# Performance work log

Measured on AMD Instinct MI355X. Metric: run time of the kernel, lower is better.

## Reference

```python
import jax, jax.numpy as jnp
import numpy as np
import math

D_MODEL = 1024
N_HEAD = 16


def setup_inputs() -> dict:
    key = jax.random.key(0)
    ks = jax.random.split(key, 5)
    x = jax.random.normal(ks[0], (2, 2048, D_MODEL), dtype=jnp.float32)
    # Linear params (torch Linear: y = x @ W.T + b); store as [in, out] for einsum
    s1 = 1.0 / math.sqrt(D_MODEL)
    W_qkv = jax.random.uniform(ks[1], (D_MODEL, 3 * D_MODEL), jnp.float32, -s1, s1)
    b_qkv = jax.random.uniform(ks[2], (3 * D_MODEL,), jnp.float32, -s1, s1)
    W_out = jax.random.uniform(ks[3], (D_MODEL, D_MODEL), jnp.float32, -s1, s1)
    b_out = jax.random.uniform(ks[4], (D_MODEL,), jnp.float32, -s1, s1)
    return {"x": x, "W_qkv": W_qkv, "b_qkv": b_qkv, "W_out": W_out, "b_out": b_out}


def reference(x, W_qkv, b_qkv, W_out, b_out):
    B, L, D = x.shape
    H = N_HEAD
    hd = D // H
    qkv = x @ W_qkv + b_qkv                      # [B, L, 3D]
    q, k, v = jnp.split(qkv, 3, axis=-1)
    # [B, H, L, hd]
    q = q.reshape(B, L, H, hd).transpose(0, 2, 1, 3)
    k = k.reshape(B, L, H, hd).transpose(0, 2, 1, 3)
    v = v.reshape(B, L, H, hd).transpose(0, 2, 1, 3)
    scale = 1.0 / math.sqrt(hd)
    scores = jnp.einsum('bhqd,bhkd->bhqk', q, k) * scale   # [B, H, L, L]
    causal = jnp.tril(jnp.ones((L, L), dtype=bool))
    scores = jnp.where(causal, scores, jnp.float32(-jnp.inf))
    probs = jax.nn.softmax(scores, axis=-1)
    out = jnp.einsum('bhqk,bhkd->bhqd', probs, v)          # [B, H, L, hd]
    out = out.transpose(0, 2, 1, 3).reshape(B, L, D)
    out = out @ W_out + b_out
    return jnp.squeeze(out)
```

## Files before the change

kernel.cpp:

```cpp
#include <hip/hip_runtime.h>
#include <hip/hip_bf16.h>

#define SEQ    2048
#define NHEAD  16
#define HD     64
#define DMODEL 1024

using bf16 = __hip_bfloat16;
using short8 = __attribute__((ext_vector_type(8))) short;
using short4v = __attribute__((ext_vector_type(4))) short;
using f32x4  = __attribute__((ext_vector_type(4))) float;

__device__ __forceinline__ float fast_exp2(float x) {
  return __builtin_amdgcn_exp2f(x);
}
#define WAIT_LGKM0() __builtin_amdgcn_s_waitcnt(0xC07F)

__device__ __forceinline__ void gload_lds16(const bf16* g, bf16* l) {
  __builtin_amdgcn_global_load_lds(
      (const __attribute__((address_space(1))) void*)g,
      (__attribute__((address_space(3))) void*)l, 16, 0, 0);
}


__global__ void prep_k(const float* __restrict__ x, bf16* __restrict__ xb,
                       const float* __restrict__ Wqkv, bf16* __restrict__ WqkvT,
                       const float* __restrict__ Wout, bf16* __restrict__ WoutT) {
  __shared__ bf16 tile[32][33];
  const int id = blockIdx.x, tid = threadIdx.x;
  if (id < 2048) {
    int i = (id * 256 + tid) * 8;
    bf16 tmp[8];
    #pragma unroll
    for (int j = 0; j < 8; ++j) tmp[j] = __float2bfloat16(x[i + j]);
    *(short8*)&xb[i] = *(short8*)tmp;
    return;
  }
  const float* in; bf16* out; int R, C, tx32, ty32;
  if (id < 2048 + 3072) {
    int t = id - 2048; in = Wqkv; out = WqkvT; R = 1024; C = 3072;
    tx32 = t % 96; ty32 = t / 96;
  } else {
    int t = id - 5120; in = Wout; out = WoutT; R = 1024; C = 1024;
    tx32 = t % 32; ty32 = t / 32;
  }
  int c0 = tx32 * 32, r0 = ty32 * 32;
  int tx = tid & 31, ty = tid >> 5;
  #pragma unroll
  for (int i = ty; i < 32; i += 8)
    tile[i][tx] = __float2bfloat16(in[(size_t)(r0 + i) * C + c0 + tx]);
  __syncthreads();
  #pragma unroll
  for (int i = ty; i < 32; i += 8)
    out[(size_t)(c0 + i) * R + r0 + tx] = tile[tx][i];
}

__global__ void transpose_v_k(const bf16* __restrict__ in, bf16* __restrict__ out) {
  __shared__ bf16 tile[32][33];
  const int bh = blockIdx.z;
  const bf16* ip = in  + (size_t)bh * SEQ * HD;
  bf16* op       = out + (size_t)bh * HD * SEQ;
  int c0 = blockIdx.x * 32, r0 = blockIdx.y * 32;
  int tx = threadIdx.x & 31, ty = threadIdx.x >> 5;
  #pragma unroll
  for (int i = ty; i < 32; i += 8)
    tile[i][tx] = ip[(size_t)(r0 + i) * HD + c0 + tx];
  __syncthreads();
  #pragma unroll
  for (int i = ty; i < 32; i += 8)
    op[(size_t)(c0 + i) * SEQ + r0 + tx] = tile[tx][i];
}

template <int MODE>
__global__ __launch_bounds__(256)
void gemm_bt(const bf16* __restrict__ A, const bf16* __restrict__ BT,
             const float* __restrict__ bias,
             bf16* __restrict__ out0, bf16* __restrict__ out1,
             bf16* __restrict__ out2, float* __restrict__ outf) {
  constexpr int K = 1024;
  __shared__ __align__(16) bf16 As[128 * 32];
  __shared__ __align__(16) bf16 Bs[128 * 32];
  const int tid = threadIdx.x;
  const int wave = tid >> 6, lane = tid & 63;
  const int quad = lane >> 4, l16 = lane & 15;
  const int waveM = (wave >> 1) * 64, waveN = (wave & 1) * 64;
  const int m0 = blockIdx.x * 128, n0 = blockIdx.y * 128;
  const int srow = (lane >> 2);
  const int scol = (((lane & 3) ^ ((lane >> 3) & 3)) * 8);
  const int q8   = (quad ^ ((l16 >> 1) & 3)) * 8;

  const f32x4 zero4 = {0.f, 0.f, 0.f, 0.f};
  f32x4 acc[4][4];
  #pragma unroll
  for (int i = 0; i < 4; ++i)
    #pragma unroll
    for (int j = 0; j < 4; ++j) acc[i][j] = zero4;

  for (int k0 = 0; k0 < K; k0 += 32) {
    __syncthreads();
    #pragma unroll
    for (int half = 0; half < 2; ++half) {
      int grow = half * 64 + wave * 16 + srow;
      gload_lds16(&A [(size_t)(m0 + grow) * K + k0 + scol],
                  &As[(half * 64 + wave * 16) * 32]);
      gload_lds16(&BT[(size_t)(n0 + grow) * K + k0 + scol],
                  &Bs[(half * 64 + wave * 16) * 32]);
    }
    __syncthreads();
    short8 af[4], bfm[4];
    #pragma unroll
    for (int mt = 0; mt < 4; ++mt)
      af[mt] = *(const short8*)&As[(waveM + mt * 16 + l16) * 32 + q8];
    #pragma unroll
    for (int nt = 0; nt < 4; ++nt)
      bfm[nt] = *(const short8*)&Bs[(waveN + nt * 16 + l16) * 32 + q8];
    #pragma unroll
    for (int mt = 0; mt < 4; ++mt)
      #pragma unroll
      for (int nt = 0; nt < 4; ++nt)
        acc[mt][nt] = __builtin_amdgcn_mfma_f32_16x16x32_bf16(
            af[mt], bfm[nt], acc[mt][nt], 0, 0, 0);
  }

  #pragma unroll
  for (int nt = 0; nt < 4; ++nt) {
    int n = n0 + waveN + nt * 16 + l16;
    float bvv = bias[n];
    #pragma unroll
    for (int mt = 0; mt < 4; ++mt) {
      #pragma unroll
      for (int r = 0; r < 4; ++r) {
        int m = m0 + waveM + mt * 16 + quad * 4 + r;
        float v = acc[mt][nt][r] + bvv;
        if (MODE == 1) {
          outf[(size_t)m * 1024 + n] = v;
        } else {
          bf16 v16 = __float2bfloat16(v);
          int which = n >> 10, oo = n & 1023;
          int h = oo >> 6, c = oo & 63;
          int b = m >> 11, l = m & 2047;
          size_t idx = ((size_t)(b * NHEAD + h) * SEQ + l) * HD + c;
          if (which == 0)      out0[idx] = v16;
          else if (which == 1) out1[idx] = v16;
          else                 out2[idx] = v16;
        }
      }
    }
  }
}

__global__ __launch_bounds__(256)
void attn_k(const bf16* __restrict__ Q, const bf16* __restrict__ Kb,
            const bf16* __restrict__ VT, bf16* __restrict__ O) {
  __shared__ __align__(16) bf16 Ks[2][2][64 * 32];
  __shared__ __align__(16) bf16 Vs[2][2][64 * 32];
  __shared__ __align__(16) bf16 Plds[4][16][72];
  const int tid = threadIdx.x;
  const int wave = tid >> 6, lane = tid & 63;
  const int quad = lane >> 4, l16 = lane & 15;
  const int srow = lane >> 2;
  const int scol = (((lane & 3) ^ ((lane >> 3) & 3)) * 8);
  const int q8   = (quad ^ ((l16 >> 1) & 3)) * 8;
  const int id = blockIdx.x;
  const int bh = id & 31, blkx = id >> 5;
  const int b = bh >> 4, h = bh & 15;

  const bf16* Qp = Q  + (size_t)bh * SEQ * HD;
  const bf16* Kp = Kb + (size_t)bh * SEQ * HD;
  const bf16* Vp = VT + (size_t)bh * HD * SEQ;

  const f32x4 zero4 = {0.f, 0.f, 0.f, 0.f};
  const float c = 0.18033688011112042f;
  const float mc = 8.0f * c;

  for (int pass = 0; pass < 2; ++pass) {
    const int qt = pass ? (31 - blkx) : blkx;
    const int q0w = qt * 64 + wave * 16;
    const int q_lane = q0w + l16;
    const int ntiles = qt + 1;

    short8 qf0 = *(const short8*)&Qp[(size_t)(q0w + l16) * HD + quad * 8];
    short8 qf1 = *(const short8*)&Qp[(size_t)(q0w + l16) * HD + 32 + quad * 8];

    f32x4 oacc[4];
    #pragma unroll
    for (int dt = 0; dt < 4; ++dt) oacc[dt] = zero4;
    float l4[4] = {0.f, 0.f, 0.f, 0.f};


    {
      const int k0 = 0;
      #pragma unroll
      for (int hh = 0; hh < 2; ++hh)
        gload_lds16(&Kp[(size_t)(k0 + wave * 16 + srow) * HD + hh * 32 + scol],
                    &Ks[0][hh][(wave * 16) * 32]);
      #pragma unroll
      for (int ch = 0; ch < 2; ++ch)
        gload_lds16(&Vp[(size_t)(wave * 16 + srow) * SEQ + k0 + ch * 32 + scol],
                    &Vs[0][ch][(wave * 16) * 32]);
    }
    __syncthreads();

    for (int t = 0; t < ntiles; ++t) {
      const int buf = t & 1;
      if (t + 1 < ntiles) {
        const int k1 = (t + 1) << 6, nb = buf ^ 1;
        #pragma unroll
        for (int hh = 0; hh < 2; ++hh)
          gload_lds16(&Kp[(size_t)(k1 + wave * 16 + srow) * HD + hh * 32 + scol],
                      &Ks[nb][hh][(wave * 16) * 32]);
        #pragma unroll
        for (int ch = 0; ch < 2; ++ch)
          gload_lds16(&Vp[(size_t)(wave * 16 + srow) * SEQ + k1 + ch * 32 + scol],
                      &Vs[nb][ch][(wave * 16) * 32]);
      }
      const int k0 = t << 6;

      f32x4 s[4];
      #pragma unroll
      for (int g = 0; g < 4; ++g) {
        short8 ka = *(const short8*)&Ks[buf][0][(g * 16 + l16) * 32 + q8];
        short8 kb = *(const short8*)&Ks[buf][1][(g * 16 + l16) * 32 + q8];
        f32x4 sg = zero4;
        sg = __builtin_amdgcn_mfma_f32_16x16x32_bf16(ka, qf0, sg, 0, 0, 0);
        sg = __builtin_amdgcn_mfma_f32_16x16x32_bf16(kb, qf1, sg, 0, 0, 0);
        s[g] = sg;
      }

      if (t == ntiles - 1) {
        #pragma unroll
        for (int g = 0; g < 4; ++g)
          #pragma unroll
          for (int r = 0; r < 4; ++r) {
            int k = k0 + g * 16 + quad * 4 + r;
            s[g][r] = (k <= q_lane) ? s[g][r] : -__builtin_inff();
          }
      }

      #pragma unroll
      for (int g = 0; g < 4; ++g) {
        bf16 pb[4];
        #pragma unroll
        for (int r = 0; r < 4; ++r) {
          float p = fast_exp2(__builtin_fmaf(s[g][r], c, -mc));
          l4[r] += p;
          pb[r] = __float2bfloat16(p);
        }
        *(short4v*)&Plds[wave][l16][g * 16 + quad * 4] = *(short4v*)pb;
      }
      WAIT_LGKM0();

      #pragma unroll
      for (int ch = 0; ch < 2; ++ch) {
        short8 pf = *(const short8*)&Plds[wave][l16][ch * 32 + quad * 8];
        #pragma unroll
        for (int dt = 0; dt < 4; ++dt) {
          short8 vf = *(const short8*)&Vs[buf][ch][(dt * 16 + l16) * 32 + q8];
          oacc[dt] = __builtin_amdgcn_mfma_f32_16x16x32_bf16(vf, pf, oacc[dt], 0, 0, 0);
        }
      }
      __syncthreads();
    }

    float l_i = (l4[0] + l4[1]) + (l4[2] + l4[3]);
    l_i += __shfl_xor(l_i, 16, 64);
    l_i += __shfl_xor(l_i, 32, 64);
    float inv = 1.f / l_i;

    #pragma unroll
    for (int dt = 0; dt < 4; ++dt) {
      bf16 ob[4];
      #pragma unroll
      for (int r = 0; r < 4; ++r) ob[r] = __float2bfloat16(oacc[dt][r] * inv);
      *(short4v*)&Plds[wave][l16][dt * 16 + quad * 4] = *(short4v*)ob;
    }
    WAIT_LGKM0();
    {
      int row = lane >> 2;
      int col = (lane & 3) * 16;
      short8 o0 = *(const short8*)&Plds[wave][row][col];
      short8 o1 = *(const short8*)&Plds[wave][row][col + 8];
      size_t base = ((size_t)(b * SEQ + q0w + row)) * DMODEL + h * HD + col;
      *(short8*)&O[base]     = o0;
      *(short8*)&O[base + 8] = o1;
    }
    WAIT_LGKM0();
  }
}

extern "C" void kernel_launch(void* const* d_in, const int* in_sizes, int n_in,
                              void* d_out, int out_size, void* d_ws, size_t ws_size,
                              hipStream_t stream) {
  const float* x    = (const float*)d_in[0];
  const float* Wqkv = (const float*)d_in[1];
  const float* bqkv = (const float*)d_in[2];
  const float* Wout = (const float*)d_in[3];
  const float* bout = (const float*)d_in[4];
  float* out = (float*)d_out;

  char* ws = (char*)d_ws;
  const size_t MB = 1024 * 1024;
  char* big    = ws + 16384;
  bf16* Kbuf   = (bf16*)(big);
  bf16* VTb    = (bf16*)(big + 8 * MB);
  bf16* xb     = (bf16*)(big + 16 * MB);
  bf16* AO     = (bf16*)(big + 16 * MB);
  bf16* WqkvT  = (bf16*)(big + 24 * MB);
  bf16* WoutT  = (bf16*)(big + 30 * MB);
  bf16* Qb     = (bf16*)d_out;
  bf16* Vtmp   = (bf16*)((char*)d_out + 8 * MB);

  prep_k<<<6144, 256, 0, stream>>>(x, xb, Wqkv, WqkvT, Wout, WoutT);
  gemm_bt<0><<<dim3(4096 / 128, 3072 / 128), 256, 0, stream>>>(
      xb, WqkvT, bqkv, Qb, Kbuf, Vtmp, nullptr);
  transpose_v_k<<<dim3(HD / 32, SEQ / 32, 32), 256, 0, stream>>>(Vtmp, VTb);
  attn_k<<<512, 256, 0, stream>>>(Qb, Kbuf, VTb, AO);
  gemm_bt<1><<<dim3(4096 / 128, 1024 / 128), 256, 0, stream>>>(
      AO, WoutT, bout, nullptr, nullptr, nullptr, out);
}
```

Measured before the change: 178.0 us.

## Fuse V transpose into QKV GEMM epilogue and split attention into one tile per block

The QKV GEMM epilogue now writes V directly in transposed [bh, hd, seq] layout with packed 4-element stores, and the Q/K tiles swap MFMA operands so they can also store 4 contiguous head-dim values. This removes the separate transpose kernel and its extra round trip through memory. The attention kernel drops its two-pass pairing of query tiles, launches 1024 blocks ordered longest-first, and sets launch bounds for 3 blocks per CU plus s_setprio around the MFMA sections. The trade-off is a less even per-block load, and the strided V writes may coalesce poorly.

```diff
diff --git a/kernel.cpp b/kernel.cpp
--- a/kernel.cpp
+++ b/kernel.cpp
@@ -53,22 +53,6 @@
   #pragma unroll
   for (int i = ty; i < 32; i += 8)
     out[(size_t)(c0 + i) * R + r0 + tx] = tile[tx][i];
-}
-
-__global__ void transpose_v_k(const bf16* __restrict__ in, bf16* __restrict__ out) {
-  __shared__ bf16 tile[32][33];
-  const int bh = blockIdx.z;
-  const bf16* ip = in  + (size_t)bh * SEQ * HD;
-  bf16* op       = out + (size_t)bh * HD * SEQ;
-  int c0 = blockIdx.x * 32, r0 = blockIdx.y * 32;
-  int tx = threadIdx.x & 31, ty = threadIdx.x >> 5;
-  #pragma unroll
-  for (int i = ty; i < 32; i += 8)
-    tile[i][tx] = ip[(size_t)(r0 + i) * HD + c0 + tx];
-  __syncthreads();
-  #pragma unroll
-  for (int i = ty; i < 32; i += 8)
-    op[(size_t)(c0 + i) * SEQ + r0 + tx] = tile[tx][i];
 }
 
 template <int MODE>
@@ -85,6 +69,7 @@
   const int quad = lane >> 4, l16 = lane & 15;
   const int waveM = (wave >> 1) * 64, waveN = (wave & 1) * 64;
   const int m0 = blockIdx.x * 128, n0 = blockIdx.y * 128;
+  const bool swapped = (MODE == 0) && (n0 < 2048);
   const int srow = (lane >> 2);
   const int scol = (((lane & 3) ^ ((lane >> 3) & 3)) * 8);
   const int q8   = (quad ^ ((l16 >> 1) & 3)) * 8;
@@ -114,42 +99,80 @@
     #pragma unroll
     for (int nt = 0; nt < 4; ++nt)
       bfm[nt] = *(const short8*)&Bs[(waveN + nt * 16 + l16) * 32 + q8];
-    #pragma unroll
-    for (int mt = 0; mt < 4; ++mt)
-      #pragma unroll
-      for (int nt = 0; nt < 4; ++nt)
-        acc[mt][nt] = __builtin_amdgcn_mfma_f32_16x16x32_bf16(
-            af[mt], bfm[nt], acc[mt][nt], 0, 0, 0);
-  }
-
-  #pragma unroll
-  for (int nt = 0; nt < 4; ++nt) {
-    int n = n0 + waveN + nt * 16 + l16;
-    float bvv = bias[n];
-    #pragma unroll
-    for (int mt = 0; mt < 4; ++mt) {
-      #pragma unroll
-      for (int r = 0; r < 4; ++r) {
-        int m = m0 + waveM + mt * 16 + quad * 4 + r;
-        float v = acc[mt][nt][r] + bvv;
-        if (MODE == 1) {
-          outf[(size_t)m * 1024 + n] = v;
-        } else {
-          bf16 v16 = __float2bfloat16(v);
-          int which = n >> 10, oo = n & 1023;
-          int h = oo >> 6, c = oo & 63;
-          int b = m >> 11, l = m & 2047;
-          size_t idx = ((size_t)(b * NHEAD + h) * SEQ + l) * HD + c;
-          if (which == 0)      out0[idx] = v16;
-          else if (which == 1) out1[idx] = v16;
-          else                 out2[idx] = v16;
+    if (swapped) {
+      #pragma unroll
+      for (int mt = 0; mt < 4; ++mt)
+        #pragma unroll
+        for (int nt = 0; nt < 4; ++nt)
+          acc[mt][nt] = __builtin_amdgcn_mfma_f32_16x16x32_bf16(
+              bfm[nt], af[mt], acc[mt][nt], 0, 0, 0);
+    } else {
+      #pragma unroll
+      for (int mt = 0; mt < 4; ++mt)
+        #pragma unroll
+        for (int nt = 0; nt < 4; ++nt)
+          acc[mt][nt] = __builtin_amdgcn_mfma_f32_16x16x32_bf16(
+              af[mt], bfm[nt], acc[mt][nt], 0, 0, 0);
+    }
+  }
+
+  if (MODE == 1) {
+    #pragma unroll
+    for (int nt = 0; nt < 4; ++nt) {
+      int n = n0 + waveN + nt * 16 + l16;
+      float bvv = bias[n];
+      #pragma unroll
+      for (int mt = 0; mt < 4; ++mt) {
+        #pragma unroll
+        for (int r = 0; r < 4; ++r) {
+          int m = m0 + waveM + mt * 16 + quad * 4 + r;
+          outf[(size_t)m * 1024 + n] = acc[mt][nt][r] + bvv;
         }
       }
     }
-  }
-}
-
-__global__ __launch_bounds__(256)
+  } else if (swapped) {
+    #pragma unroll
+    for (int nt = 0; nt < 4; ++nt) {
+      int nb = n0 + waveN + nt * 16 + quad * 4;
+      const f32x4 b4 = *(const f32x4*)&bias[nb];
+      int oo = nb & 1023;
+      int h = oo >> 6, cc = oo & 63;
+      bf16* outp = (nb >> 10) ? out1 : out0;
+      #pragma unroll
+      for (int mt = 0; mt < 4; ++mt) {
+        int m = m0 + waveM + mt * 16 + l16;
+        int bb = m >> 11, l = m & 2047;
+        bf16 tmp[4];
+        #pragma unroll
+        for (int r = 0; r < 4; ++r)
+          tmp[r] = __float2bfloat16(acc[mt][nt][r] + b4[r]);
+        *(short4v*)&outp[((size_t)(bb * NHEAD + h) * SEQ + l) * HD + cc] =
+            *(short4v*)tmp;
+      }
+    }
+  } else {
+    #pragma unroll
+    for (int nt = 0; nt < 4; ++nt) {
+      int n = n0 + waveN + nt * 16 + l16;
+      float bvv = bias[n];
+      int oo = n & 1023;
+      int h = oo >> 6, cc = oo & 63;
+      #pragma unroll
+      for (int mt = 0; mt < 4; ++mt) {
+        int m = m0 + waveM + mt * 16 + quad * 4;
+        int bb = m >> 11, l = m & 2047;
+        bf16 tmp[4];
+        #pragma unroll
+        for (int r = 0; r < 4; ++r)
+          tmp[r] = __float2bfloat16(acc[mt][nt][r] + bvv);
+        *(short4v*)&out2[((size_t)(bb * NHEAD + h) * HD + cc) * SEQ + l] =
+            *(short4v*)tmp;
+      }
+    }
+  }
+}
+
+__global__ __launch_bounds__(256, 3)
 void attn_k(const bf16* __restrict__ Q, const bf16* __restrict__ Kb,
             const bf16* __restrict__ VT, bf16* __restrict__ O) {
   __shared__ __align__(16) bf16 Ks[2][2][64 * 32];
@@ -162,7 +185,8 @@
   const int scol = (((lane & 3) ^ ((lane >> 3) & 3)) * 8);
   const int q8   = (quad ^ ((l16 >> 1) & 3)) * 8;
   const int id = blockIdx.x;
-  const int bh = id & 31, blkx = id >> 5;
+  const int bh = id & 31;
+  const int qt = 31 - (id >> 5);
   const int b = bh >> 4, h = bh & 15;
 
   const bf16* Qp = Q  + (size_t)bh * SEQ * HD;
@@ -173,118 +197,117 @@
   const float c = 0.18033688011112042f;
   const float mc = 8.0f * c;
 
-  for (int pass = 0; pass < 2; ++pass) {
-    const int qt = pass ? (31 - blkx) : blkx;
-    const int q0w = qt * 64 + wave * 16;
-    const int q_lane = q0w + l16;
-    const int ntiles = qt + 1;
-
-    short8 qf0 = *(const short8*)&Qp[(size_t)(q0w + l16) * HD + quad * 8];
-    short8 qf1 = *(const short8*)&Qp[(size_t)(q0w + l16) * HD + 32 + quad * 8];
-
-    f32x4 oacc[4];
-    #pragma unroll
-    for (int dt = 0; dt < 4; ++dt) oacc[dt] = zero4;
-    float l4[4] = {0.f, 0.f, 0.f, 0.f};
-
-
-    {
-      const int k0 = 0;
+  const int q0w = qt * 64 + wave * 16;
+  const int q_lane = q0w + l16;
+  const int ntiles = qt + 1;
+
+  short8 qf0 = *(const short8*)&Qp[(size_t)(q0w + l16) * HD + quad * 8];
+  short8 qf1 = *(const short8*)&Qp[(size_t)(q0w + l16) * HD + 32 + quad * 8];
+
+  f32x4 oacc[4];
+  #pragma unroll
+  for (int dt = 0; dt < 4; ++dt) oacc[dt] = zero4;
+  float l4[4] = {0.f, 0.f, 0.f, 0.f};
+
+  {
+    const int k0 = 0;
+    #pragma unroll
+    for (int hh = 0; hh < 2; ++hh)
+      gload_lds16(&Kp[(size_t)(k0 + wave * 16 + srow) * HD + hh * 32 + scol],
+                  &Ks[0][hh][(wave * 16) * 32]);
+    #pragma unroll
+    for (int ch = 0; ch < 2; ++ch)
+      gload_lds16(&Vp[(size_t)(wave * 16 + srow) * SEQ + k0 + ch * 32 + scol],
+                  &Vs[0][ch][(wave * 16) * 32]);
+  }
+  __syncthreads();
+
+  for (int t = 0; t < ntiles; ++t) {
+    const int buf = t & 1;
+    if (t + 1 < ntiles) {
+      const int k1 = (t + 1) << 6, nb = buf ^ 1;
       #pragma unroll
       for (int hh = 0; hh < 2; ++hh)
-        gload_lds16(&Kp[(size_t)(k0 + wave * 16 + srow) * HD + hh * 32 + scol],
-                    &Ks[0][hh][(wave * 16) * 32]);
+        gload_lds16(&Kp[(size_t)(k1 + wave * 16 + srow) * HD + hh * 32 + scol],
+                    &Ks[nb][hh][(wave * 16) * 32]);
       #pragma unroll
       for (int ch = 0; ch < 2; ++ch)
-        gload_lds16(&Vp[(size_t)(wave * 16 + srow) * SEQ + k0 + ch * 32 + scol],
-                    &Vs[0][ch][(wave * 16) * 32]);
-    }
+        gload_lds16(&Vp[(size_t)(wave * 16 + srow) * SEQ + k1 + ch * 32 + scol],
+                    &Vs[nb][ch][(wave * 16) * 32]);
+    }
+    const int k0 = t << 6;
+
+    f32x4 s[4];
+    __builtin_amdgcn_s_setprio(1);
+    #pragma unroll
+    for (int g = 0; g < 4; ++g) {
+      short8 ka = *(const short8*)&Ks[buf][0][(g * 16 + l16) * 32 + q8];
+      short8 kb = *(const short8*)&Ks[buf][1][(g * 16 + l16) * 32 + q8];
+      f32x4 sg = zero4;
+      sg = __builtin_amdgcn_mfma_f32_16x16x32_bf16(ka, qf0, sg, 0, 0, 0);
+      sg = __builtin_amdgcn_mfma_f32_16x16x32_bf16(kb, qf1, sg, 0, 0, 0);
+      s[g] = sg;
+    }
+    __builtin_amdgcn_s_setprio(0);
+
+    if (t == ntiles - 1) {
+      #pragma unroll
+      for (int g = 0; g < 4; ++g)
+        #pragma unroll
+        for (int r = 0; r < 4; ++r) {
+          int k = k0 + g * 16 + quad * 4 + r;
+          s[g][r] = (k <= q_lane) ? s[g][r] : -__builtin_inff();
+        }
+    }
+
+    #pragma unroll
+    for (int g = 0; g < 4; ++g) {
+      bf16 pb[4];
+      #pragma unroll
+      for (int r = 0; r < 4; ++r) {
+        float p = fast_exp2(__builtin_fmaf(s[g][r], c, -mc));
+        l4[r] += p;
+        pb[r] = __float2bfloat16(p);
+      }
+      *(short4v*)&Plds[wave][l16][g * 16 + quad * 4] = *(short4v*)pb;
+    }
+    WAIT_LGKM0();
+
+    __builtin_amdgcn_s_setprio(1);
+    #pragma unroll
+    for (int ch = 0; ch < 2; ++ch) {
+      short8 pf = *(const short8*)&Plds[wave][l16][ch * 32 + quad * 8];
+      #pragma unroll
+      for (int dt = 0; dt < 4; ++dt) {
+        short8 vf = *(const short8*)&Vs[buf][ch][(dt * 16 + l16) * 32 + q8];
+        oacc[dt] = __builtin_amdgcn_mfma_f32_16x16x32_bf16(vf, pf, oacc[dt], 0, 0, 0);
+      }
+    }
+    __builtin_amdgcn_s_setprio(0);
     __syncthreads();
-
-    for (int t = 0; t < ntiles; ++t) {
-      const int buf = t & 1;
-      if (t + 1 < ntiles) {
-        const int k1 = (t + 1) << 6, nb = buf ^ 1;
-        #pragma unroll
-        for (int hh = 0; hh < 2; ++hh)
-          gload_lds16(&Kp[(size_t)(k1 + wave * 16 + srow) * HD + hh * 32 + scol],
-                      &Ks[nb][hh][(wave * 16) * 32]);
-        #pragma unroll
-        for (int ch = 0; ch < 2; ++ch)
-          gload_lds16(&Vp[(size_t)(wave * 16 + srow) * SEQ + k1 + ch * 32 + scol],
-                      &Vs[nb][ch][(wave * 16) * 32]);
-      }
-      const int k0 = t << 6;
-
-      f32x4 s[4];
-      #pragma unroll
-      for (int g = 0; g < 4; ++g) {
-        short8 ka = *(const short8*)&Ks[buf][0][(g * 16 + l16) * 32 + q8];
-        short8 kb = *(const short8*)&Ks[buf][1][(g * 16 + l16) * 32 + q8];
-        f32x4 sg = zero4;
-        sg = __builtin_amdgcn_mfma_f32_16x16x32_bf16(ka, qf0, sg, 0, 0, 0);
-        sg = __builtin_amdgcn_mfma_f32_16x16x32_bf16(kb, qf1, sg, 0, 0, 0);
-        s[g] = sg;
-      }
-
-      if (t == ntiles - 1) {
-        #pragma unroll
-        for (int g = 0; g < 4; ++g)
-          #pragma unroll
-          for (int r = 0; r < 4; ++r) {
-            int k = k0 + g * 16 + quad * 4 + r;
-            s[g][r] = (k <= q_lane) ? s[g][r] : -__builtin_inff();
-          }
-      }
-
-      #pragma unroll
-      for (int g = 0; g < 4; ++g) {
-        bf16 pb[4];
-        #pragma unroll
-        for (int r = 0; r < 4; ++r) {
-          float p = fast_exp2(__builtin_fmaf(s[g][r], c, -mc));
-          l4[r] += p;
-          pb[r] = __float2bfloat16(p);
-        }
-        *(short4v*)&Plds[wave][l16][g * 16 + quad * 4] = *(short4v*)pb;
-      }
-      WAIT_LGKM0();
-
-      #pragma unroll
-      for (int ch = 0; ch < 2; ++ch) {
-        short8 pf = *(const short8*)&Plds[wave][l16][ch * 32 + quad * 8];
-        #pragma unroll
-        for (int dt = 0; dt < 4; ++dt) {
-          short8 vf = *(const short8*)&Vs[buf][ch][(dt * 16 + l16) * 32 + q8];
-          oacc[dt] = __builtin_amdgcn_mfma_f32_16x16x32_bf16(vf, pf, oacc[dt], 0, 0, 0);
-        }
-      }
-      __syncthreads();
-    }
-
-    float l_i = (l4[0] + l4[1]) + (l4[2] + l4[3]);
-    l_i += __shfl_xor(l_i, 16, 64);
-    l_i += __shfl_xor(l_i, 32, 64);
-    float inv = 1.f / l_i;
-
-    #pragma unroll
-    for (int dt = 0; dt < 4; ++dt) {
-      bf16 ob[4];
-      #pragma unroll
-      for (int r = 0; r < 4; ++r) ob[r] = __float2bfloat16(oacc[dt][r] * inv);
-      *(short4v*)&Plds[wave][l16][dt * 16 + quad * 4] = *(short4v*)ob;
-    }
-    WAIT_LGKM0();
-    {
-      int row = lane >> 2;
-      int col = (lane & 3) * 16;
-      short8 o0 = *(const short8*)&Plds[wave][row][col];
-      short8 o1 = *(const short8*)&Plds[wave][row][col + 8];
-      size_t base = ((size_t)(b * SEQ + q0w + row)) * DMODEL + h * HD + col;
-      *(short8*)&O[base]     = o0;
-      *(short8*)&O[base + 8] = o1;
-    }
-    WAIT_LGKM0();
+  }
+
+  float l_i = (l4[0] + l4[1]) + (l4[2] + l4[3]);
+  l_i += __shfl_xor(l_i, 16, 64);
+  l_i += __shfl_xor(l_i, 32, 64);
+  float inv = 1.f / l_i;
+
+  #pragma unroll
+  for (int dt = 0; dt < 4; ++dt) {
+    bf16 ob[4];
+    #pragma unroll
+    for (int r = 0; r < 4; ++r) ob[r] = __float2bfloat16(oacc[dt][r] * inv);
+    *(short4v*)&Plds[wave][l16][dt * 16 + quad * 4] = *(short4v*)ob;
+  }
+  WAIT_LGKM0();
+  {
+    int row = lane >> 2;
+    int col = (lane & 3) * 16;
+    short8 o0 = *(const short8*)&Plds[wave][row][col];
+    short8 o1 = *(const short8*)&Plds[wave][row][col + 8];
+    size_t base = ((size_t)(b * SEQ + q0w + row)) * DMODEL + h * HD + col;
+    *(short8*)&O[base]     = o0;
+    *(short8*)&O[base + 8] = o1;
   }
 }
 
@@ -308,13 +331,11 @@
   bf16* WqkvT  = (bf16*)(big + 24 * MB);
   bf16* WoutT  = (bf16*)(big + 30 * MB);
   bf16* Qb     = (bf16*)d_out;
-  bf16* Vtmp   = (bf16*)((char*)d_out + 8 * MB);
 
   prep_k<<<6144, 256, 0, stream>>>(x, xb, Wqkv, WqkvT, Wout, WoutT);
   gemm_bt<0><<<dim3(4096 / 128, 3072 / 128), 256, 0, stream>>>(
-      xb, WqkvT, bqkv, Qb, Kbuf, Vtmp, nullptr);
-  transpose_v_k<<<dim3(HD / 32, SEQ / 32, 32), 256, 0, stream>>>(Vtmp, VTb);
-  attn_k<<<512, 256, 0, stream>>>(Qb, Kbuf, VTb, AO);
+      xb, WqkvT, bqkv, Qb, Kbuf, VTb, nullptr);
+  attn_k<<<1024, 256, 0, stream>>>(Qb, Kbuf, VTb, AO);
   gemm_bt<1><<<dim3(4096 / 128, 1024 / 128), 256, 0, stream>>>(
       AO, WoutT, bout, nullptr, nullptr, nullptr, out);
 }
```

After: 184.4 us. +3.6%, slower.

## Widen attention query tile to 128 rows per block, two 16-row groups per wave

Applied to the files above, without the earlier changes.

Each wave now processes 32 query rows as two MFMA groups, so every K/V tile loaded into LDS is reused across 128 queries instead of 64. This halves K/V traffic per query. Because the number of q-tiles halves, the two-pass causal load balancing is replaced by a single pass with heavy tiles scheduled first. s_setprio hints around the MFMA sections and a launch bound of 2 blocks per CU are added. The costs are higher register pressure and coarser load balance across blocks.

```diff
diff --git a/kernel.cpp b/kernel.cpp
--- a/kernel.cpp
+++ b/kernel.cpp
@@ -149,12 +149,12 @@
   }
 }
 
-__global__ __launch_bounds__(256)
+__global__ __launch_bounds__(256, 2)
 void attn_k(const bf16* __restrict__ Q, const bf16* __restrict__ Kb,
             const bf16* __restrict__ VT, bf16* __restrict__ O) {
   __shared__ __align__(16) bf16 Ks[2][2][64 * 32];
   __shared__ __align__(16) bf16 Vs[2][2][64 * 32];
-  __shared__ __align__(16) bf16 Plds[4][16][72];
+  __shared__ __align__(16) bf16 Plds[4][2][16][72];
   const int tid = threadIdx.x;
   const int wave = tid >> 6, lane = tid & 63;
   const int quad = lane >> 4, l16 = lane & 15;
@@ -162,7 +162,8 @@
   const int scol = (((lane & 3) ^ ((lane >> 3) & 3)) * 8);
   const int q8   = (quad ^ ((l16 >> 1) & 3)) * 8;
   const int id = blockIdx.x;
-  const int bh = id & 31, blkx = id >> 5;
+  const int bh = id & 31;
+  const int qt = 15 - (id >> 5);
   const int b = bh >> 4, h = bh & 15;
 
   const bf16* Qp = Q  + (size_t)bh * SEQ * HD;
@@ -173,118 +174,138 @@
   const float c = 0.18033688011112042f;
   const float mc = 8.0f * c;
 
-  for (int pass = 0; pass < 2; ++pass) {
-    const int qt = pass ? (31 - blkx) : blkx;
-    const int q0w = qt * 64 + wave * 16;
-    const int q_lane = q0w + l16;
-    const int ntiles = qt + 1;
-
-    short8 qf0 = *(const short8*)&Qp[(size_t)(q0w + l16) * HD + quad * 8];
-    short8 qf1 = *(const short8*)&Qp[(size_t)(q0w + l16) * HD + 32 + quad * 8];
-
-    f32x4 oacc[4];
-    #pragma unroll
-    for (int dt = 0; dt < 4; ++dt) oacc[dt] = zero4;
-    float l4[4] = {0.f, 0.f, 0.f, 0.f};
-
-
-    {
-      const int k0 = 0;
+  const int q0w = qt * 128 + wave * 32;
+  const int ntiles = 2 * qt + 2;
+
+  short8 qf[2][2];
+  #pragma unroll
+  for (int g = 0; g < 2; ++g) {
+    qf[g][0] = *(const short8*)&Qp[(size_t)(q0w + g * 16 + l16) * HD + quad * 8];
+    qf[g][1] = *(const short8*)&Qp[(size_t)(q0w + g * 16 + l16) * HD + 32 + quad * 8];
+  }
+
+  f32x4 oacc[2][4];
+  #pragma unroll
+  for (int g = 0; g < 2; ++g)
+    #pragma unroll
+    for (int dt = 0; dt < 4; ++dt) oacc[g][dt] = zero4;
+  float l4[2][4] = {{0.f, 0.f, 0.f, 0.f}, {0.f, 0.f, 0.f, 0.f}};
+
+  {
+    #pragma unroll
+    for (int hh = 0; hh < 2; ++hh)
+      gload_lds16(&Kp[(size_t)(wave * 16 + srow) * HD + hh * 32 + scol],
+                  &Ks[0][hh][(wave * 16) * 32]);
+    #pragma unroll
+    for (int ch = 0; ch < 2; ++ch)
+      gload_lds16(&Vp[(size_t)(wave * 16 + srow) * SEQ + ch * 32 + scol],
+                  &Vs[0][ch][(wave * 16) * 32]);
+  }
+  __syncthreads();
+
+  for (int t = 0; t < ntiles; ++t) {
+    const int buf = t & 1;
+    if (t + 1 < ntiles) {
+      const int k1 = (t + 1) << 6, nb = buf ^ 1;
       #pragma unroll
       for (int hh = 0; hh < 2; ++hh)
-        gload_lds16(&Kp[(size_t)(k0 + wave * 16 + srow) * HD + hh * 32 + scol],
-                    &Ks[0][hh][(wave * 16) * 32]);
+        gload_lds16(&Kp[(size_t)(k1 + wave * 16 + srow) * HD + hh * 32 + scol],
+                    &Ks[nb][hh][(wave * 16) * 32]);
       #pragma unroll
       for (int ch = 0; ch < 2; ++ch)
-        gload_lds16(&Vp[(size_t)(wave * 16 + srow) * SEQ + k0 + ch * 32 + scol],
-                    &Vs[0][ch][(wave * 16) * 32]);
-    }
-    __syncthreads();
-
-    for (int t = 0; t < ntiles; ++t) {
-      const int buf = t & 1;
-      if (t + 1 < ntiles) {
-        const int k1 = (t + 1) << 6, nb = buf ^ 1;
+        gload_lds16(&Vp[(size_t)(wave * 16 + srow) * SEQ + k1 + ch * 32 + scol],
+                    &Vs[nb][ch][(wave * 16) * 32]);
+    }
+    const int k0 = t << 6;
+
+    f32x4 s[2][4];
+    __builtin_amdgcn_s_setprio(1);
+    #pragma unroll
+    for (int g4 = 0; g4 < 4; ++g4) {
+      short8 ka = *(const short8*)&Ks[buf][0][(g4 * 16 + l16) * 32 + q8];
+      short8 kb = *(const short8*)&Ks[buf][1][(g4 * 16 + l16) * 32 + q8];
+      #pragma unroll
+      for (int g = 0; g < 2; ++g) {
+        f32x4 sg = zero4;
+        sg = __builtin_amdgcn_mfma_f32_16x16x32_bf16(ka, qf[g][0], sg, 0, 0, 0);
+        sg = __builtin_amdgcn_mfma_f32_16x16x32_bf16(kb, qf[g][1], sg, 0, 0, 0);
+        s[g][g4] = sg;
+      }
+    }
+    __builtin_amdgcn_s_setprio(0);
+
+    if (t >= ntiles - 2) {
+      #pragma unroll
+      for (int g = 0; g < 2; ++g) {
+        const int q_lane = q0w + g * 16 + l16;
         #pragma unroll
-        for (int hh = 0; hh < 2; ++hh)
-          gload_lds16(&Kp[(size_t)(k1 + wave * 16 + srow) * HD + hh * 32 + scol],
-                      &Ks[nb][hh][(wave * 16) * 32]);
-        #pragma unroll
-        for (int ch = 0; ch < 2; ++ch)
-          gload_lds16(&Vp[(size_t)(wave * 16 + srow) * SEQ + k1 + ch * 32 + scol],
-                      &Vs[nb][ch][(wave * 16) * 32]);
-      }
-      const int k0 = t << 6;
-
-      f32x4 s[4];
-      #pragma unroll
-      for (int g = 0; g < 4; ++g) {
-        short8 ka = *(const short8*)&Ks[buf][0][(g * 16 + l16) * 32 + q8];
-        short8 kb = *(const short8*)&Ks[buf][1][(g * 16 + l16) * 32 + q8];
-        f32x4 sg = zero4;
-        sg = __builtin_amdgcn_mfma_f32_16x16x32_bf16(ka, qf0, sg, 0, 0, 0);
-        sg = __builtin_amdgcn_mfma_f32_16x16x32_bf16(kb, qf1, sg, 0, 0, 0);
-        s[g] = sg;
-      }
-
-      if (t == ntiles - 1) {
-        #pragma unroll
-        for (int g = 0; g < 4; ++g)
+        for (int g4 = 0; g4 < 4; ++g4)
           #pragma unroll
           for (int r = 0; r < 4; ++r) {
-            int k = k0 + g * 16 + quad * 4 + r;
-            s[g][r] = (k <= q_lane) ? s[g][r] : -__builtin_inff();
+            int k = k0 + g4 * 16 + quad * 4 + r;
+            s[g][g4][r] = (k <= q_lane) ? s[g][g4][r] : -__builtin_inff();
           }
       }
-
-      #pragma unroll
-      for (int g = 0; g < 4; ++g) {
+    }
+
+    #pragma unroll
+    for (int g = 0; g < 2; ++g)
+      #pragma unroll
+      for (int g4 = 0; g4 < 4; ++g4) {
         bf16 pb[4];
         #pragma unroll
         for (int r = 0; r < 4; ++r) {
-          float p = fast_exp2(__builtin_fmaf(s[g][r], c, -mc));
-          l4[r] += p;
+          float p = fast_exp2(__builtin_fmaf(s[g][g4][r], c, -mc));
+          l4[g][r] += p;
           pb[r] = __float2bfloat16(p);
         }
-        *(short4v*)&Plds[wave][l16][g * 16 + quad * 4] = *(short4v*)pb;
-      }
-      WAIT_LGKM0();
-
-      #pragma unroll
-      for (int ch = 0; ch < 2; ++ch) {
-        short8 pf = *(const short8*)&Plds[wave][l16][ch * 32 + quad * 8];
-        #pragma unroll
-        for (int dt = 0; dt < 4; ++dt) {
-          short8 vf = *(const short8*)&Vs[buf][ch][(dt * 16 + l16) * 32 + q8];
-          oacc[dt] = __builtin_amdgcn_mfma_f32_16x16x32_bf16(vf, pf, oacc[dt], 0, 0, 0);
-        }
-      }
-      __syncthreads();
-    }
-
-    float l_i = (l4[0] + l4[1]) + (l4[2] + l4[3]);
+        *(short4v*)&Plds[wave][g][l16][g4 * 16 + quad * 4] = *(short4v*)pb;
+      }
+    WAIT_LGKM0();
+
+    __builtin_amdgcn_s_setprio(1);
+    #pragma unroll
+    for (int ch = 0; ch < 2; ++ch) {
+      short8 pf0 = *(const short8*)&Plds[wave][0][l16][ch * 32 + quad * 8];
+      short8 pf1 = *(const short8*)&Plds[wave][1][l16][ch * 32 + quad * 8];
+      #pragma unroll
+      for (int dt = 0; dt < 4; ++dt) {
+        short8 vf = *(const short8*)&Vs[buf][ch][(dt * 16 + l16) * 32 + q8];
+        oacc[0][dt] = __builtin_amdgcn_mfma_f32_16x16x32_bf16(vf, pf0, oacc[0][dt], 0, 0, 0);
+        oacc[1][dt] = __builtin_amdgcn_mfma_f32_16x16x32_bf16(vf, pf1, oacc[1][dt], 0, 0, 0);
+      }
+    }
+    __builtin_amdgcn_s_setprio(0);
+    __syncthreads();
+  }
+
+  #pragma unroll
+  for (int g = 0; g < 2; ++g) {
+    float l_i = (l4[g][0] + l4[g][1]) + (l4[g][2] + l4[g][3]);
     l_i += __shfl_xor(l_i, 16, 64);
     l_i += __shfl_xor(l_i, 32, 64);
     float inv = 1.f / l_i;
-
     #pragma unroll
     for (int dt = 0; dt < 4; ++dt) {
       bf16 ob[4];
       #pragma unroll
-      for (int r = 0; r < 4; ++r) ob[r] = __float2bfloat16(oacc[dt][r] * inv);
-      *(short4v*)&Plds[wave][l16][dt * 16 + quad * 4] = *(short4v*)ob;
-    }
-    WAIT_LGKM0();
-    {
-      int row = lane >> 2;
-      int col = (lane & 3) * 16;
-      short8 o0 = *(const short8*)&Plds[wave][row][col];
-      short8 o1 = *(const short8*)&Plds[wave][row][col + 8];
-      size_t base = ((size_t)(b * SEQ + q0w + row)) * DMODEL + h * HD + col;
+      for (int r = 0; r < 4; ++r) ob[r] = __float2bfloat16(oacc[g][dt][r] * inv);
+      *(short4v*)&Plds[wave][g][l16][dt * 16 + quad * 4] = *(short4v*)ob;
+    }
+  }
+  WAIT_LGKM0();
+  {
+    int row = lane >> 2;
+    int col = (lane & 3) * 16;
+    #pragma unroll
+    for (int g = 0; g < 2; ++g) {
+      short8 o0 = *(const short8*)&Plds[wave][g][row][col];
+      short8 o1 = *(const short8*)&Plds[wave][g][row][col + 8];
+      size_t base =
+          ((size_t)(b * SEQ + q0w + g * 16 + row)) * DMODEL + h * HD + col;
       *(short8*)&O[base]     = o0;
       *(short8*)&O[base + 8] = o1;
     }
-    WAIT_LGKM0();
   }
 }
 
```

Result: slower. 186.5 us (+4.8%).
